# Kernel tuning notes

Hardware: AMD Instinct MI355X
Metric: run time of the kernel (lower is better)

The kernel has to match this reference:

```python
import jax, jax.numpy as jnp
import numpy as np

MIN_NORM = 1e-15
PROJ_EPS = 4e-3   # HGCN PoincareBall eps for float32
C = 1.0
N_NODES = 100000
DEG = 5
F_IN = 128


def _artanh(x):
    return jnp.arctanh(jnp.clip(x, -1.0 + 1e-7, 1.0 - 1e-7))


def _norm(x):
    # clamped L2 norm over last dim, keepdims
    return jnp.maximum(jnp.sqrt(jnp.sum(x * x, axis=-1, keepdims=True)), MIN_NORM)


def proj(x, c):
    norm = _norm(x)
    maxnorm = (1.0 - PROJ_EPS) / jnp.sqrt(c)
    return jnp.where(norm > maxnorm, x / norm * maxnorm, x)


def expmap0(u, c):
    sc = jnp.sqrt(c)
    un = _norm(u)
    return jnp.tanh(sc * un) * u / (sc * un)


def logmap0(p, c):
    sc = jnp.sqrt(c)
    pn = _norm(p)
    return p / pn / sc * _artanh(sc * pn)


def mobius_matvec(m, x, c):
    # HGCN convention: mx = x @ m^T
    sc = jnp.sqrt(c)
    x_norm = _norm(x)
    mx = x @ m.T
    mx_norm = _norm(mx)
    res = jnp.tanh(mx_norm / x_norm * _artanh(sc * x_norm)) * mx / (mx_norm * sc)
    zero = jnp.all(mx == 0, axis=-1, keepdims=True)
    return jnp.where(zero, jnp.zeros_like(res), res)


def setup_inputs() -> dict:
    key = jax.random.key(0)
    k1, k2, k3, k4 = jax.random.split(key, 4)
    x = jax.random.normal(k1, (N_NODES, F_IN), jnp.float32) * 0.1
    gain = 1.414
    W = jax.random.normal(k2, (F_IN, F_IN), jnp.float32) * gain * np.sqrt(2.0 / (F_IN + F_IN))
    a = jax.random.normal(k3, (1, 2 * F_IN), jnp.float32) * gain * np.sqrt(2.0 / (1 + 2 * F_IN))
    # edge list: every node has DEG out-edges so row-sum normalization is safe
    src = jnp.repeat(jnp.arange(N_NODES, dtype=jnp.int32), DEG)
    dst = jax.random.randint(k4, (N_NODES * DEG,), 0, N_NODES, jnp.int32)
    edge = jnp.stack([src, dst])  # [2, E]
    return {"x": x, "edge": edge, "W": W, "a": a}


def reference(x, edge, W, a):
    c = C
    N = x.shape[0]
    # h = logmap0(proj(mobius_matvec(x, W)))  -> [F, N] (module's transposed layout)
    h = logmap0(proj(mobius_matvec(x, W, c), c), c)
    src, dst = edge[0], edge[1]
    # per-edge gather: [2F, E]
    edge_h = jnp.concatenate([h[:, src], h[:, dst]], axis=0)
    edge_h = proj(expmap0(edge_h, c), c)
    # mobius_matvec(edge_h.T, a) -> a @ edge_h : [1, E] -> [E]
    ee = jnp.squeeze(mobius_matvec(edge_h.T, a, c))
    ee = logmap0(proj(ee, c), c)
    ee = jnp.exp(-jax.nn.gelu(ee, approximate=False))  # positive edge weights
    # sparse spmm row-sum and aggregation (scatter-add by source node)
    e_rowsum = jax.ops.segment_sum(ee, src, num_segments=N)                     # [N]
    h_prime = jax.ops.segment_sum(ee[:, None] * h.T[dst], src, num_segments=N)  # [N, F]
    h_prime = h_prime / e_rowsum[:, None]
    return proj(expmap0(jax.nn.elu(h_prime), c), c)
```

## Files before the change

kernel.cpp:

```cpp
#include <hip/hip_runtime.h>
#include <math.h>

#define F 128
#define DEG 5
#define TM 128
#define MAXNORM_D 0.996
#define MIN_NORM_D 1e-15

typedef float f32x4 __attribute__((ext_vector_type(4)));
typedef short s16x8 __attribute__((ext_vector_type(8)));
typedef _Float16 f16x4 __attribute__((ext_vector_type(4)));

__device__ inline double atanh_clip(double v) {
    v = fmin(fmax(v, -1.0 + 1e-7), 1.0 - 1e-7);
    return atanh(v);
}

__device__ inline void load_lds16(const void* g, void* l) {
    __builtin_amdgcn_global_load_lds((const __attribute__((address_space(1))) void*)g,
                                     (__attribute__((address_space(3))) void*)l, 16, 0, 0);
}

__device__ inline void split2(float v0, float v1, unsigned& hi, unsigned& lo) {
    unsigned b0 = __float_as_uint(v0), b1 = __float_as_uint(v1);
    unsigned h0 = (b0 + 0x8000u) >> 16;
    unsigned h1 = (b1 + 0x8000u) >> 16;
    float l0 = v0 - __uint_as_float(h0 << 16);
    float l1 = v1 - __uint_as_float(h1 << 16);
    hi = h0 | (h1 << 16);
    lo = (__float_as_uint(l0) >> 16) | (__float_as_uint(l1) & 0xFFFF0000u);
}

__global__ __launch_bounds__(256) void k_ph(const float* __restrict__ W,
                                            uint4* __restrict__ Wfh, uint4* __restrict__ Wfl,
                                            const int* __restrict__ edge, int* __restrict__ cnt, int E) {
    if (blockIdx.x < 8) {
        int tid = blockIdx.x * 256 + threadIdx.x;
        int c = tid >> 9;
        int tp = (tid >> 6) & 7;
        int lane = tid & 63;
        int f = tp * 16 + (lane & 15);
        int k = c * 32 + (lane >> 4) * 8;
        const float* wp = W + f * F + k;
        unsigned h[4], l[4];
#pragma unroll
        for (int p = 0; p < 4; p++) split2(wp[2 * p], wp[2 * p + 1], h[p], l[p]);
        Wfh[tid] = make_uint4(h[0], h[1], h[2], h[3]);
        Wfl[tid] = make_uint4(l[0], l[1], l[2], l[3]);
    } else {
        int stride = (gridDim.x - 8) * 256;
        for (int e = (blockIdx.x - 8) * 256 + threadIdx.x; e < E; e += stride)
            atomicAdd(&cnt[edge[E + e]], 1);
    }
}

__global__ __launch_bounds__(512, 4) void k_gemm(const float* __restrict__ x,
                                                 const uint4* __restrict__ Wfh, const uint4* __restrict__ Wfl,
                                                 const int* __restrict__ cnt, float* __restrict__ y,
                                                 float* __restrict__ ssum2, float* __restrict__ wsum2, int N) {
    __shared__ uint4 Wh_s[2048];
    __shared__ uint4 Wl_s[2048];
    __shared__ float red_ss[F];
    __shared__ float red_ws[F];
    __shared__ int cntL[TM];

    int t = threadIdx.x;
    int lane = t & 63;
    int w = t >> 6;
    int n0 = blockIdx.x * TM;

    if (t < F) { red_ss[t] = 0.f; red_ws[t] = 0.f; }
    if (t < TM) { int n = n0 + t; cntL[t] = (n < N) ? cnt[n] : 0; }

#pragma unroll
    for (int r = 0; r < 4; r++) {
        int off = (r * 512 + t) * 16;
        load_lds16((const char*)Wfh + off, (char*)Wh_s + off);
    }
#pragma unroll
    for (int r = 0; r < 4; r++) {
        int off = (r * 512 + t) * 16;
        load_lds16((const char*)Wfl + off, (char*)Wl_s + off);
    }

    int row = n0 + w * 16 + (lane & 15);
    if (row > N - 1) row = N - 1;
    const float* xr = x + (size_t)row * F + (lane >> 4) * 8;

    float4 av0[4], av1[4];
#pragma unroll
    for (int c = 0; c < 4; c++) {
        av0[c] = *(const float4*)(xr + c * 32);
        av1[c] = *(const float4*)(xr + c * 32 + 4);
    }

    f32x4 acc[8];
#pragma unroll
    for (int i = 0; i < 8; i++) acc[i] = (f32x4){0.f, 0.f, 0.f, 0.f};

    __syncthreads();

#pragma unroll
    for (int c = 0; c < 4; c++) {
        unsigned h[4], l[4];
        split2(av0[c].x, av0[c].y, h[0], l[0]);
        split2(av0[c].z, av0[c].w, h[1], l[1]);
        split2(av1[c].x, av1[c].y, h[2], l[2]);
        split2(av1[c].z, av1[c].w, h[3], l[3]);
        s16x8 a_hi = __builtin_bit_cast(s16x8, make_uint4(h[0], h[1], h[2], h[3]));
        s16x8 a_lo = __builtin_bit_cast(s16x8, make_uint4(l[0], l[1], l[2], l[3]));
#pragma unroll
        for (int tp = 0; tp < 8; tp++) {
            s16x8 bh = __builtin_bit_cast(s16x8, Wh_s[(c * 8 + tp) * 64 + lane]);
            s16x8 bl = __builtin_bit_cast(s16x8, Wl_s[(c * 8 + tp) * 64 + lane]);
            acc[tp] = __builtin_amdgcn_mfma_f32_16x16x32_bf16(a_hi, bh, acc[tp], 0, 0, 0);
            acc[tp] = __builtin_amdgcn_mfma_f32_16x16x32_bf16(a_lo, bh, acc[tp], 0, 0, 0);
            acc[tp] = __builtin_amdgcn_mfma_f32_16x16x32_bf16(a_hi, bl, acc[tp], 0, 0, 0);
        }
    }

    int fb = lane & 15;
    int rg = lane >> 4;
#pragma unroll
    for (int tp = 0; tp < 8; tp++) {
        int f = tp * 16 + fb;
        float sv = 0.f, wv = 0.f;
#pragma unroll
        for (int r = 0; r < 4; r++) {
            int lr = w * 16 + rg * 4 + r;
            int n = n0 + lr;
            float v = acc[tp][r];
            if (n < N) {
                y[(size_t)n * F + f] = v;
                sv += v * v;
                wv += (float)cntL[lr] * v * v;
            }
        }
        sv += __shfl_xor(sv, 16, 64); sv += __shfl_xor(sv, 32, 64);
        wv += __shfl_xor(wv, 16, 64); wv += __shfl_xor(wv, 32, 64);
        if (lane < 16) {
            atomicAdd(&red_ss[f], sv);
            atomicAdd(&red_ws[f], wv);
        }
    }
    __syncthreads();
    if (t < F) {
        int bank = (blockIdx.x & 7) * F;
        atomicAdd(&ssum2[bank + t], red_ss[t]);
        atomicAdd(&wsum2[bank + t], red_ws[t]);
    }
}

__global__ __launch_bounds__(256) void k_scalars(const float* __restrict__ W, const float* __restrict__ a,
                                                 const float* __restrict__ ssum2, const float* __restrict__ wsum2,
                                                 float* __restrict__ s_arr, float* __restrict__ asrc,
                                                 float* __restrict__ adst, double* __restrict__ an_out) {
    int t = threadIdx.x;
    double av = (double)a[t];
    av *= av;
#pragma unroll
    for (int off = 32; off; off >>= 1) av += __shfl_down(av, off, 64);
    __shared__ double wred[4];
    if ((t & 63) == 0) wred[t >> 6] = av;
    __syncthreads();
    double an = fmax(sqrt(wred[0] + wred[1] + wred[2] + wred[3]), MIN_NORM_D);
    if (t == 0) an_out[0] = an;

    if (t < F) {
        float ss2f = 0.f, ws2f = 0.f;
#pragma unroll
        for (int b = 0; b < 8; b++) { ss2f += ssum2[b * F + t]; ws2f += wsum2[b * F + t]; }

        double wn2 = 0.0;
        for (int k = 0; k < F; k++) { double w = (double)W[t * F + k]; wn2 += w * w; }
        double wn = fmax(sqrt(wn2), MIN_NORM_D);
        double mxnf = fmax(sqrt((double)ss2f), MIN_NORM_D);
        double tt = tanh(mxnf / wn * atanh_clip(wn));
        double rn = fmax(tt, MIN_NORM_D);
        double pf = (rn > MAXNORM_D) ? MAXNORM_D / rn : 1.0;
        double pn = rn * pf;
        double s = (tt / mxnf) * pf * atanh_clip(pn) / pn;
        s_arr[t] = (float)s;

        double un_s = fmax(s * sqrt((double)DEG * (double)ss2f), MIN_NORM_D);
        double th_s = tanh(un_s);
        double rn2 = fmax(th_s, MIN_NORM_D);
        double pf2 = (rn2 > MAXNORM_D) ? MAXNORM_D / rn2 : 1.0;
        double q_s = s * (th_s / un_s) * pf2;
        asrc[t] = (float)((double)a[t] * q_s);

        double un_d = fmax(s * sqrt((double)ws2f), MIN_NORM_D);
        double th_d = tanh(un_d);
        double rn3 = fmax(th_d, MIN_NORM_D);
        double pf3 = (rn3 > MAXNORM_D) ? MAXNORM_D / rn3 : 1.0;
        double q_d = s * (th_d / un_d) * pf3;
        adst[t] = (float)((double)a[F + t] * q_d);
    }
}

__global__ __launch_bounds__(256) void k_pq(const float* __restrict__ y, const float* __restrict__ asrc,
                                            const float* __restrict__ adst, float* __restrict__ P,
                                            float* __restrict__ Q, _Float16* __restrict__ yh, int N) {
    __shared__ float as4[F], ad4[F];
    int t = threadIdx.x;
    if (t < F) { as4[t] = asrc[t]; ad4[t] = adst[t]; }
    __syncthreads();
    int lane = t & 31;
    float4 av = *(const float4*)&as4[lane * 4];
    float4 bv = *(const float4*)&ad4[lane * 4];
    for (int nb = blockIdx.x * 8; nb < N; nb += gridDim.x * 8) {
        int n = nb + (t >> 5);
        if (n < N) {
            float4 yv = *(const float4*)&y[(size_t)n * F + lane * 4];
            f16x4 hv = { (_Float16)yv.x, (_Float16)yv.y, (_Float16)yv.z, (_Float16)yv.w };
            *(f16x4*)&yh[(size_t)n * F + lane * 4] = hv;
            float p = yv.x * av.x + yv.y * av.y + yv.z * av.z + yv.w * av.w;
            float q = yv.x * bv.x + yv.y * bv.y + yv.z * bv.z + yv.w * bv.w;
#pragma unroll
            for (int off = 16; off; off >>= 1) {
                p += __shfl_down(p, off, 32);
                q += __shfl_down(q, off, 32);
            }
            if (lane == 0) { P[n] = p; Q[n] = q; }
        }
    }
}

__global__ __launch_bounds__(256) void k_edge(const int* __restrict__ edge, const float* __restrict__ P,
                                              const float* __restrict__ Q, float* __restrict__ ee_pre,
                                              double* __restrict__ mxn2, int E) {
    int t = threadIdx.x;
    double local = 0.0;
    for (int e0 = blockIdx.x * 256; e0 < E; e0 += gridDim.x * 256) {
        int e = e0 + t;
        if (e < E) {
            int s = e / DEG;
            int d = edge[E + e];
            float v = P[s] + Q[d];
            ee_pre[e] = v;
            local += (double)v * (double)v;
        }
    }
#pragma unroll
    for (int off = 32; off; off >>= 1) local += __shfl_down(local, off, 64);
    __shared__ double wsum[4];
    if ((t & 63) == 0) wsum[t >> 6] = local;
    __syncthreads();
    if (t == 0) atomicAdd(mxn2, wsum[0] + wsum[1] + wsum[2] + wsum[3]);
}

__global__ __launch_bounds__(256) void k_wagg(const int* __restrict__ edge, const _Float16* __restrict__ yh,
                                              const float* __restrict__ ee_pre,
                                              const double* __restrict__ an_p, const double* __restrict__ mxn2_p,
                                              const float* __restrict__ s_arr,
                                              float* __restrict__ out, int N, int E) {
    __shared__ float gS;
    int t = threadIdx.x;
    if (t == 0) {
        double an = an_p[0];
        double mxn = fmax(sqrt(mxn2_p[0]), MIN_NORM_D);
        double t2 = tanh(mxn / an * atanh_clip(an));
        double f2 = t2 / mxn;
        double rnp = fmax(t2, MIN_NORM_D);
        double pfp = (rnp > MAXNORM_D) ? MAXNORM_D / rnp : 1.0;
        double pnp = rnp * pfp;
        gS = (float)(f2 * pfp * atanh_clip(pnp) / pnp);
    }
    __syncthreads();
    float g = gS;

    int lane = t & 63;
    int sub = lane & 7;
    int slot = t >> 3;
    int gbase = lane & ~7;

    int n = blockIdx.x * 32 + slot;
    bool active = (n < N);
    int nc = active ? n : N - 1;

    float w = 0.f; int d = 0;
    if (sub < DEG) {
        int e = nc * DEG + sub;
        float xg = g * ee_pre[e];
        float gl = 0.5f * xg * (1.f + erff(xg * 0.70710678f));
        w = expf(-gl);
        d = edge[E + e] << 7;
    }
    float wj[DEG]; int dj[DEG];
#pragma unroll
    for (int j = 0; j < DEG; j++) {
        wj[j] = __shfl(w, gbase + j, 64);
        dj[j] = __shfl(d, gbase + j, 64);
    }
    float rowsum = wj[0] + wj[1] + wj[2] + wj[3] + wj[4];
    float inv = 1.f / rowsum;

    float4 acc[4];
#pragma unroll
    for (int p = 0; p < 4; p++) acc[p] = make_float4(0.f, 0.f, 0.f, 0.f);
#pragma unroll
    for (int j = 0; j < DEG; j++) {
        const _Float16* yp = yh + dj[j] + sub * 4;
        float wv = wj[j];
#pragma unroll
        for (int p = 0; p < 4; p++) {
            f16x4 hv = *(const f16x4*)(yp + p * 32);
            acc[p].x = fmaf(wv, (float)hv[0], acc[p].x);
            acc[p].y = fmaf(wv, (float)hv[1], acc[p].y);
            acc[p].z = fmaf(wv, (float)hv[2], acc[p].z);
            acc[p].w = fmaf(wv, (float)hv[3], acc[p].w);
        }
    }

    float4 s4[4];
#pragma unroll
    for (int p = 0; p < 4; p++) s4[p] = *(const float4*)&s_arr[p * 32 + sub * 4];

    float4 el[4];
    float ss = 0.f;
#pragma unroll
    for (int p = 0; p < 4; p++) {
        float h;
        h = s4[p].x * acc[p].x * inv; el[p].x = (h > 0.f) ? h : expm1f(h);
        h = s4[p].y * acc[p].y * inv; el[p].y = (h > 0.f) ? h : expm1f(h);
        h = s4[p].z * acc[p].z * inv; el[p].z = (h > 0.f) ? h : expm1f(h);
        h = s4[p].w * acc[p].w * inv; el[p].w = (h > 0.f) ? h : expm1f(h);
        ss += el[p].x * el[p].x + el[p].y * el[p].y + el[p].z * el[p].z + el[p].w * el[p].w;
    }
    ss += __shfl_xor(ss, 1, 64);
    ss += __shfl_xor(ss, 2, 64);
    ss += __shfl_xor(ss, 4, 64);

    float un = fmaxf(sqrtf(ss), 1e-15f);
    float th = tanhf(un);
    float sc = th / un;
    float rn = fmaxf(th, 1e-15f);
    if (rn > 0.996f) sc *= 0.996f / rn;
    if (active) {
        float* op = out + (size_t)n * F + sub * 4;
#pragma unroll
        for (int p = 0; p < 4; p++) {
            float4 o = make_float4(el[p].x * sc, el[p].y * sc, el[p].z * sc, el[p].w * sc);
            *(float4*)(op + p * 32) = o;
        }
    }
}

extern "C" void kernel_launch(void* const* d_in, const int* in_sizes, int n_in,
                              void* d_out, int out_size, void* d_ws, size_t ws_size,
                              hipStream_t stream) {
    const float* x = (const float*)d_in[0];
    const int* edge = (const int*)d_in[1];
    const float* W = (const float*)d_in[2];
    const float* a = (const float*)d_in[3];
    float* out = (float*)d_out;
    int N = in_sizes[0] / F;
    int E = in_sizes[1] / 2;

    char* ws = (char*)d_ws;
    size_t off = 0;
    float* y = (float*)(ws + off);       off += (size_t)N * F * 4;
    _Float16* yh = (_Float16*)(ws + off); off += (size_t)N * F * 2;
    uint4* Wfh = (uint4*)(ws + off);     off += 2048 * 16;
    uint4* Wfl = (uint4*)(ws + off);     off += 2048 * 16;
    float* ee_pre = (float*)(ws + off);  off += (size_t)E * 4;
    float* P = (float*)(ws + off);       off += (size_t)N * 4;
    float* Q = (float*)(ws + off);       off += (size_t)N * 4;
    char* zbase = ws + off;
    int* cnt = (int*)(ws + off);         off += (size_t)N * 4;
    float* ssum2 = (float*)(ws + off);   off += 8 * F * 4;
    float* wsum2 = (float*)(ws + off);   off += 8 * F * 4;
    double* mxn2 = (double*)(ws + off);  off += 8;
    size_t zlen = (size_t)((ws + off) - zbase);
    double* an_p = (double*)(ws + off);  off += 8;
    float* s_arr = (float*)(ws + off);   off += 512;
    float* asrc = (float*)(ws + off);    off += 512;
    float* adst = (float*)(ws + off);    off += 512;

    hipMemsetAsync(zbase, 0, zlen, stream);
    k_ph<<<8 + 1024, 256, 0, stream>>>(W, Wfh, Wfl, edge, cnt, E);
    k_gemm<<<(N + TM - 1) / TM, 512, 0, stream>>>(x, Wfh, Wfl, cnt, y, ssum2, wsum2, N);
    k_scalars<<<1, 256, 0, stream>>>(W, a, ssum2, wsum2, s_arr, asrc, adst, an_p);
    k_pq<<<2048, 256, 0, stream>>>(y, asrc, adst, P, Q, yh, N);
    k_edge<<<1024, 256, 0, stream>>>(edge, P, Q, ee_pre, mxn2, E);
    k_wagg<<<(N + 31) / 32, 256, 0, stream>>>(edge, yh, ee_pre, an_p, mxn2, s_arr, out, N, E);
}
```

Baseline: 210.6 us.

## Write fp16 GEMM output directly and recompute edge logits in aggregation

```diff
diff --git a/kernel.cpp b/kernel.cpp
--- a/kernel.cpp
+++ b/kernel.cpp
@@ -56,7 +56,7 @@
 
 __global__ __launch_bounds__(512, 4) void k_gemm(const float* __restrict__ x,
                                                  const uint4* __restrict__ Wfh, const uint4* __restrict__ Wfl,
-                                                 const int* __restrict__ cnt, float* __restrict__ y,
+                                                 const int* __restrict__ cnt, _Float16* __restrict__ yh,
                                                  float* __restrict__ ssum2, float* __restrict__ wsum2, int N) {
     __shared__ uint4 Wh_s[2048];
     __shared__ uint4 Wl_s[2048];
@@ -121,6 +121,8 @@
 
     int fb = lane & 15;
     int rg = lane >> 4;
+    int odd = fb & 1;
+
 #pragma unroll
     for (int tp = 0; tp < 8; tp++) {
         int f = tp * 16 + fb;
@@ -131,7 +133,6 @@
             int n = n0 + lr;
             float v = acc[tp][r];
             if (n < N) {
-                y[(size_t)n * F + f] = v;
                 sv += v * v;
                 wv += (float)cntL[lr] * v * v;
             }
@@ -143,6 +144,32 @@
             atomicAdd(&red_ws[f], wv);
         }
     }
+
+#pragma unroll
+    for (int r = 0; r < 4; r++) {
+        int n = n0 + w * 16 + rg * 4 + r;
+        unsigned hb[8], ob[8], pk[8];
+#pragma unroll
+        for (int tp = 0; tp < 8; tp++) {
+            _Float16 hv = (_Float16)acc[tp][r];
+            hb[tp] = (unsigned)__builtin_bit_cast(unsigned short, hv);
+        }
+#pragma unroll
+        for (int tp = 0; tp < 8; tp++) ob[tp] = (unsigned)__shfl_xor((int)hb[tp], 1, 64);
+#pragma unroll
+        for (int tp = 0; tp < 8; tp++)
+            pk[tp] = odd ? (ob[tp] | (hb[tp] << 16)) : (hb[tp] | (ob[tp] << 16));
+        if (n < N) {
+            unsigned* bp = (unsigned*)(yh + (size_t)n * F + (fb & ~1));
+#pragma unroll
+            for (int i = 0; i < 4; i++) {
+                int tp = 2 * i + odd;
+                unsigned v = odd ? pk[2 * i + 1] : pk[2 * i];
+                bp[tp * 8] = v;
+            }
+        }
+    }
+
     __syncthreads();
     if (t < F) {
         int bank = (blockIdx.x & 7) * F;
@@ -198,9 +225,9 @@
     }
 }
 
-__global__ __launch_bounds__(256) void k_pq(const float* __restrict__ y, const float* __restrict__ asrc,
+__global__ __launch_bounds__(256) void k_pq(const _Float16* __restrict__ yh, const float* __restrict__ asrc,
                                             const float* __restrict__ adst, float* __restrict__ P,
-                                            float* __restrict__ Q, _Float16* __restrict__ yh, int N) {
+                                            float* __restrict__ Q, int N) {
     __shared__ float as4[F], ad4[F];
     int t = threadIdx.x;
     if (t < F) { as4[t] = asrc[t]; ad4[t] = adst[t]; }
@@ -211,9 +238,8 @@
     for (int nb = blockIdx.x * 8; nb < N; nb += gridDim.x * 8) {
         int n = nb + (t >> 5);
         if (n < N) {
-            float4 yv = *(const float4*)&y[(size_t)n * F + lane * 4];
-            f16x4 hv = { (_Float16)yv.x, (_Float16)yv.y, (_Float16)yv.z, (_Float16)yv.w };
-            *(f16x4*)&yh[(size_t)n * F + lane * 4] = hv;
+            f16x4 hv = *(const f16x4*)&yh[(size_t)n * F + lane * 4];
+            float4 yv = make_float4((float)hv[0], (float)hv[1], (float)hv[2], (float)hv[3]);
             float p = yv.x * av.x + yv.y * av.y + yv.z * av.z + yv.w * av.w;
             float q = yv.x * bv.x + yv.y * bv.y + yv.z * bv.z + yv.w * bv.w;
 #pragma unroll
@@ -227,17 +253,14 @@
 }
 
 __global__ __launch_bounds__(256) void k_edge(const int* __restrict__ edge, const float* __restrict__ P,
-                                              const float* __restrict__ Q, float* __restrict__ ee_pre,
+                                              const float* __restrict__ Q,
                                               double* __restrict__ mxn2, int E) {
     int t = threadIdx.x;
     double local = 0.0;
     for (int e0 = blockIdx.x * 256; e0 < E; e0 += gridDim.x * 256) {
         int e = e0 + t;
         if (e < E) {
-            int s = e / DEG;
-            int d = edge[E + e];
-            float v = P[s] + Q[d];
-            ee_pre[e] = v;
+            float v = P[e / DEG] + Q[edge[E + e]];
             local += (double)v * (double)v;
         }
     }
@@ -250,7 +273,7 @@
 }
 
 __global__ __launch_bounds__(256) void k_wagg(const int* __restrict__ edge, const _Float16* __restrict__ yh,
-                                              const float* __restrict__ ee_pre,
+                                              const float* __restrict__ P, const float* __restrict__ Q,
                                               const double* __restrict__ an_p, const double* __restrict__ mxn2_p,
                                               const float* __restrict__ s_arr,
                                               float* __restrict__ out, int N, int E) {
@@ -281,10 +304,12 @@
     float w = 0.f; int d = 0;
     if (sub < DEG) {
         int e = nc * DEG + sub;
-        float xg = g * ee_pre[e];
+        int dn = edge[E + e];
+        float v = P[nc] + Q[dn];
+        float xg = g * v;
         float gl = 0.5f * xg * (1.f + erff(xg * 0.70710678f));
         w = expf(-gl);
-        d = edge[E + e] << 7;
+        d = dn << 7;
     }
     float wj[DEG]; int dj[DEG];
 #pragma unroll
@@ -359,11 +384,9 @@
 
     char* ws = (char*)d_ws;
     size_t off = 0;
-    float* y = (float*)(ws + off);       off += (size_t)N * F * 4;
     _Float16* yh = (_Float16*)(ws + off); off += (size_t)N * F * 2;
     uint4* Wfh = (uint4*)(ws + off);     off += 2048 * 16;
     uint4* Wfl = (uint4*)(ws + off);     off += 2048 * 16;
-    float* ee_pre = (float*)(ws + off);  off += (size_t)E * 4;
     float* P = (float*)(ws + off);       off += (size_t)N * 4;
     float* Q = (float*)(ws + off);       off += (size_t)N * 4;
     char* zbase = ws + off;
@@ -379,9 +402,9 @@
 
     hipMemsetAsync(zbase, 0, zlen, stream);
     k_ph<<<8 + 1024, 256, 0, stream>>>(W, Wfh, Wfl, edge, cnt, E);
-    k_gemm<<<(N + TM - 1) / TM, 512, 0, stream>>>(x, Wfh, Wfl, cnt, y, ssum2, wsum2, N);
+    k_gemm<<<(N + TM - 1) / TM, 512, 0, stream>>>(x, Wfh, Wfl, cnt, yh, ssum2, wsum2, N);
     k_scalars<<<1, 256, 0, stream>>>(W, a, ssum2, wsum2, s_arr, asrc, adst, an_p);
-    k_pq<<<2048, 256, 0, stream>>>(y, asrc, adst, P, Q, yh, N);
-    k_edge<<<1024, 256, 0, stream>>>(edge, P, Q, ee_pre, mxn2, E);
-    k_wagg<<<(N + 31) / 32, 256, 0, stream>>>(edge, yh, ee_pre, an_p, mxn2, s_arr, out, N, E);
-}
+    k_pq<<<2048, 256, 0, stream>>>(yh, asrc, adst, P, Q, N);
+    k_edge<<<1024, 256, 0, stream>>>(edge, P, Q, mxn2, E);
+    k_wagg<<<(N + 31) / 32, 256, 0, stream>>>(edge, yh, P, Q, an_p, mxn2, s_arr, out, N, E);
+}
```

Measured after the change: 212.9 us. No clear change (+1.1%).
